# Optimization experiments

Measured on AMD Instinct MI355X. Metric: run time of the kernel, lower is better.

## Reference

```python
import jax, jax.numpy as jnp
import numpy as np

B, N, D = 64, 576, 768   # batch, num_patches (24x24), embed_dim
K = 1024                 # n_pairs
NUM_TARGETS = 2


def setup_inputs() -> dict:
    key = jax.random.key(0)
    k1, k2, k3, k4 = jax.random.split(key, 4)
    z = jax.random.normal(k1, (B, N, D), dtype=jnp.float32)
    indices = jax.random.randint(k2, (B, K, 2), 0, N, dtype=jnp.int64)
    # head params: nn.Linear(2*embed_dim, num_targets)
    W = jax.random.normal(k3, (2 * D, NUM_TARGETS), dtype=jnp.float32) * 0.02
    b_head = jax.random.normal(k4, (NUM_TARGETS,), dtype=jnp.float32) * 0.02
    return {"z": z, "indices": indices, "W": W, "b_head": b_head}


def reference(z, indices, W, b_head):
    b, n, d = z.shape
    k = indices.shape[1]
    # index_pairs: gather both patches of each pair -> [b, k, 2, d]
    batch_idx = jnp.arange(b)[:, None, None]            # [b,1,1]
    z_pairs = z[batch_idx, indices]                     # [b, k, 2, d]
    # pairwise_mlp head: concat pair along feature dim, tiny linear
    out = z_pairs.reshape(b, k, 2 * d) @ W + b_head     # [b, k, num_targets]
    return out, indices
```

## Files before the change

### kernel.cpp

```cpp
#include <hip/hip_runtime.h>

#define BB 64
#define NN 576
#define DD 768
#define KK 1024
#define ROWS (BB * NN)
#define PAIRS (BB * KK)

__device__ float4 g_P[ROWS];

__global__ __launch_bounds__(256) void partvit_proj(const float* __restrict__ z,
                                                    const float* __restrict__ W) {
    const int lane = threadIdx.x & 63;
    const int wid  = blockIdx.x * (blockDim.x >> 6) + (threadIdx.x >> 6);
    const int nw   = gridDim.x * (blockDim.x >> 6);

    const float2* __restrict__ W2 = (const float2*)W;
    float2 wa[3][4], wb[3][4];
#pragma unroll
    for (int j = 0; j < 3; ++j) {
#pragma unroll
        for (int c = 0; c < 4; ++c) {
            const int d = j * 256 + (lane << 2) + c;
            wa[j][c] = W2[d];
            wb[j][c] = W2[d + 768];
        }
    }

    const float4* __restrict__ z4 = (const float4*)z;

    for (int r = wid; r < ROWS; r += nw) {
        float a00 = 0.f, a01 = 0.f, a10 = 0.f, a11 = 0.f;
#pragma unroll
        for (int j = 0; j < 3; ++j) {
            const float4 v = z4[r * 192 + j * 64 + lane];
            a00 = fmaf(v.x, wa[j][0].x, a00);
            a00 = fmaf(v.y, wa[j][1].x, a00);
            a00 = fmaf(v.z, wa[j][2].x, a00);
            a00 = fmaf(v.w, wa[j][3].x, a00);
            a01 = fmaf(v.x, wa[j][0].y, a01);
            a01 = fmaf(v.y, wa[j][1].y, a01);
            a01 = fmaf(v.z, wa[j][2].y, a01);
            a01 = fmaf(v.w, wa[j][3].y, a01);
            a10 = fmaf(v.x, wb[j][0].x, a10);
            a10 = fmaf(v.y, wb[j][1].x, a10);
            a10 = fmaf(v.z, wb[j][2].x, a10);
            a10 = fmaf(v.w, wb[j][3].x, a10);
            a11 = fmaf(v.x, wb[j][0].y, a11);
            a11 = fmaf(v.y, wb[j][1].y, a11);
            a11 = fmaf(v.z, wb[j][2].y, a11);
            a11 = fmaf(v.w, wb[j][3].y, a11);
        }
#pragma unroll
        for (int off = 32; off > 0; off >>= 1) {
            a00 += __shfl_xor(a00, off, 64);
            a01 += __shfl_xor(a01, off, 64);
            a10 += __shfl_xor(a10, off, 64);
            a11 += __shfl_xor(a11, off, 64);
        }
        if (lane == 0) g_P[r] = make_float4(a00, a01, a10, a11);
    }
}

__global__ __launch_bounds__(256) void partvit_pairs(const int* __restrict__ idx,
                                                     const float* __restrict__ bh,
                                                     float* __restrict__ out) {
    const int t = blockIdx.x * blockDim.x + threadIdx.x;
    if (t >= PAIRS) return;
    const int2 id = ((const int2*)idx)[t];
    const int i0 = min(max(id.x, 0), NN - 1);
    const int i1 = min(max(id.y, 0), NN - 1);
    const int b = t >> 10;
    const float4 p0 = g_P[b * NN + i0];
    const float4 p1 = g_P[b * NN + i1];
    const float b0 = bh[0], b1 = bh[1];
    ((float2*)out)[t] = make_float2(p0.x + p1.z + b0, p0.y + p1.w + b1);
    ((float2*)out)[PAIRS + t] = make_float2((float)id.x, (float)id.y);
}

extern "C" void kernel_launch(void* const* d_in, const int* in_sizes, int n_in,
                              void* d_out, int out_size, void* d_ws, size_t ws_size,
                              hipStream_t stream) {
    const float* z   = (const float*)d_in[0];
    const int*   idx = (const int*)d_in[1];
    const float* W   = (const float*)d_in[2];
    const float* bh  = (const float*)d_in[3];
    float*       out = (float*)d_out;
    (void)d_ws; (void)ws_size;

    partvit_proj<<<1536, 256, 0, stream>>>(z, W);
    partvit_pairs<<<PAIRS / 256, 256, 0, stream>>>(idx, bh, out);
}
```

Baseline: 169.2 us.

## Fuse projection and pair gather into one per-batch kernel using shared memory

Result: slower. 188.0 us (+11.1%).

```diff
diff --git a/kernel.cpp b/kernel.cpp
--- a/kernel.cpp
+++ b/kernel.cpp
@@ -7,13 +7,15 @@
 #define ROWS (BB * NN)
 #define PAIRS (BB * KK)
 
-__device__ float4 g_P[ROWS];
-
-__global__ __launch_bounds__(256) void partvit_proj(const float* __restrict__ z,
-                                                    const float* __restrict__ W) {
+__global__ __launch_bounds__(1024) void partvit_fused(const float* __restrict__ z,
+                                                      const int* __restrict__ idx,
+                                                      const float* __restrict__ W,
+                                                      const float* __restrict__ bh,
+                                                      float* __restrict__ out) {
+    __shared__ float4 P[NN];
+    const int b    = blockIdx.x;
     const int lane = threadIdx.x & 63;
-    const int wid  = blockIdx.x * (blockDim.x >> 6) + (threadIdx.x >> 6);
-    const int nw   = gridDim.x * (blockDim.x >> 6);
+    const int wave = threadIdx.x >> 6;
 
     const float2* __restrict__ W2 = (const float2*)W;
     float2 wa[3][4], wb[3][4];
@@ -23,33 +25,57 @@
         for (int c = 0; c < 4; ++c) {
             const int d = j * 256 + (lane << 2) + c;
             wa[j][c] = W2[d];
-            wb[j][c] = W2[d + 768];
+            wb[j][c] = W2[d + DD];
         }
     }
 
-    const float4* __restrict__ z4 = (const float4*)z;
+    const float4* __restrict__ z4 = (const float4*)z + (size_t)b * NN * 192;
 
-    for (int r = wid; r < ROWS; r += nw) {
+    for (int r = wave; r < NN; r += 32) {
+        const int r2 = r + 16;
+        float4 v0[3], v1[3];
+#pragma unroll
+        for (int j = 0; j < 3; ++j) v0[j] = z4[r  * 192 + j * 64 + lane];
+#pragma unroll
+        for (int j = 0; j < 3; ++j) v1[j] = z4[r2 * 192 + j * 64 + lane];
+
         float a00 = 0.f, a01 = 0.f, a10 = 0.f, a11 = 0.f;
+        float c00 = 0.f, c01 = 0.f, c10 = 0.f, c11 = 0.f;
 #pragma unroll
         for (int j = 0; j < 3; ++j) {
-            const float4 v = z4[r * 192 + j * 64 + lane];
-            a00 = fmaf(v.x, wa[j][0].x, a00);
-            a00 = fmaf(v.y, wa[j][1].x, a00);
-            a00 = fmaf(v.z, wa[j][2].x, a00);
-            a00 = fmaf(v.w, wa[j][3].x, a00);
-            a01 = fmaf(v.x, wa[j][0].y, a01);
-            a01 = fmaf(v.y, wa[j][1].y, a01);
-            a01 = fmaf(v.z, wa[j][2].y, a01);
-            a01 = fmaf(v.w, wa[j][3].y, a01);
-            a10 = fmaf(v.x, wb[j][0].x, a10);
-            a10 = fmaf(v.y, wb[j][1].x, a10);
-            a10 = fmaf(v.z, wb[j][2].x, a10);
-            a10 = fmaf(v.w, wb[j][3].x, a10);
-            a11 = fmaf(v.x, wb[j][0].y, a11);
-            a11 = fmaf(v.y, wb[j][1].y, a11);
-            a11 = fmaf(v.z, wb[j][2].y, a11);
-            a11 = fmaf(v.w, wb[j][3].y, a11);
+            a00 = fmaf(v0[j].x, wa[j][0].x, a00);
+            a00 = fmaf(v0[j].y, wa[j][1].x, a00);
+            a00 = fmaf(v0[j].z, wa[j][2].x, a00);
+            a00 = fmaf(v0[j].w, wa[j][3].x, a00);
+            a01 = fmaf(v0[j].x, wa[j][0].y, a01);
+            a01 = fmaf(v0[j].y, wa[j][1].y, a01);
+            a01 = fmaf(v0[j].z, wa[j][2].y, a01);
+            a01 = fmaf(v0[j].w, wa[j][3].y, a01);
+            a10 = fmaf(v0[j].x, wb[j][0].x, a10);
+            a10 = fmaf(v0[j].y, wb[j][1].x, a10);
+            a10 = fmaf(v0[j].z, wb[j][2].x, a10);
+            a10 = fmaf(v0[j].w, wb[j][3].x, a10);
+            a11 = fmaf(v0[j].x, wb[j][0].y, a11);
+            a11 = fmaf(v0[j].y, wb[j][1].y, a11);
+            a11 = fmaf(v0[j].z, wb[j][2].y, a11);
+            a11 = fmaf(v0[j].w, wb[j][3].y, a11);
+
+            c00 = fmaf(v1[j].x, wa[j][0].x, c00);
+            c00 = fmaf(v1[j].y, wa[j][1].x, c00);
+            c00 = fmaf(v1[j].z, wa[j][2].x, c00);
+            c00 = fmaf(v1[j].w, wa[j][3].x, c00);
+            c01 = fmaf(v1[j].x, wa[j][0].y, c01);
+            c01 = fmaf(v1[j].y, wa[j][1].y, c01);
+            c01 = fmaf(v1[j].z, wa[j][2].y, c01);
+            c01 = fmaf(v1[j].w, wa[j][3].y, c01);
+            c10 = fmaf(v1[j].x, wb[j][0].x, c10);
+            c10 = fmaf(v1[j].y, wb[j][1].x, c10);
+            c10 = fmaf(v1[j].z, wb[j][2].x, c10);
+            c10 = fmaf(v1[j].w, wb[j][3].x, c10);
+            c11 = fmaf(v1[j].x, wb[j][0].y, c11);
+            c11 = fmaf(v1[j].y, wb[j][1].y, c11);
+            c11 = fmaf(v1[j].z, wb[j][2].y, c11);
+            c11 = fmaf(v1[j].w, wb[j][3].y, c11);
         }
 #pragma unroll
         for (int off = 32; off > 0; off >>= 1) {
@@ -57,22 +83,25 @@
             a01 += __shfl_xor(a01, off, 64);
             a10 += __shfl_xor(a10, off, 64);
             a11 += __shfl_xor(a11, off, 64);
+            c00 += __shfl_xor(c00, off, 64);
+            c01 += __shfl_xor(c01, off, 64);
+            c10 += __shfl_xor(c10, off, 64);
+            c11 += __shfl_xor(c11, off, 64);
         }
-        if (lane == 0) g_P[r] = make_float4(a00, a01, a10, a11);
+        if (lane == 0) {
+            P[r]  = make_float4(a00, a01, a10, a11);
+            P[r2] = make_float4(c00, c01, c10, c11);
+        }
     }
-}
 
-__global__ __launch_bounds__(256) void partvit_pairs(const int* __restrict__ idx,
-                                                     const float* __restrict__ bh,
-                                                     float* __restrict__ out) {
-    const int t = blockIdx.x * blockDim.x + threadIdx.x;
-    if (t >= PAIRS) return;
+    __syncthreads();
+
+    const int t = b * KK + (int)threadIdx.x;
     const int2 id = ((const int2*)idx)[t];
     const int i0 = min(max(id.x, 0), NN - 1);
     const int i1 = min(max(id.y, 0), NN - 1);
-    const int b = t >> 10;
-    const float4 p0 = g_P[b * NN + i0];
-    const float4 p1 = g_P[b * NN + i1];
+    const float4 p0 = P[i0];
+    const float4 p1 = P[i1];
     const float b0 = bh[0], b1 = bh[1];
     ((float2*)out)[t] = make_float2(p0.x + p1.z + b0, p0.y + p1.w + b1);
     ((float2*)out)[PAIRS + t] = make_float2((float)id.x, (float)id.y);
@@ -86,8 +115,7 @@
     const float* W   = (const float*)d_in[2];
     const float* bh  = (const float*)d_in[3];
     float*       out = (float*)d_out;
-    (void)d_ws; (void)ws_size;
+    (void)d_ws; (void)ws_size; (void)in_sizes; (void)n_in; (void)out_size;
 
-    partvit_proj<<<1536, 256, 0, stream>>>(z, W);
-    partvit_pairs<<<PAIRS / 256, 256, 0, stream>>>(idx, bh, out);
+    partvit_fused<<<BB, 1024, 0, stream>>>(z, idx, W, bh, out);
 }
```

## Fuse projection and pair gather into one kernel computing per-pair dot products

Applied to the files above, without the earlier changes.

New measurement: 187.2 us. +10.7%, slower.

```diff
diff --git a/kernel.cpp b/kernel.cpp
--- a/kernel.cpp
+++ b/kernel.cpp
@@ -7,75 +7,86 @@
 #define ROWS (BB * NN)
 #define PAIRS (BB * KK)
 
-__device__ float4 g_P[ROWS];
+#define NBLK 8192
+#define TPB  256
+#define PPB  8
 
-__global__ __launch_bounds__(256) void partvit_proj(const float* __restrict__ z,
-                                                    const float* __restrict__ W) {
+__global__ __launch_bounds__(TPB, 4)
+void partvit_direct(const float* __restrict__ z,
+                    const int* __restrict__ idx,
+                    const float* __restrict__ W,
+                    const float* __restrict__ bh,
+                    float* __restrict__ out) {
     const int lane = threadIdx.x & 63;
-    const int wid  = blockIdx.x * (blockDim.x >> 6) + (threadIdx.x >> 6);
-    const int nw   = gridDim.x * (blockDim.x >> 6);
+    const int wv   = threadIdx.x >> 6;
+
+    const int g  = (blockIdx.x & 7) * (NBLK / 8) + (blockIdx.x >> 3);
+    const int p0 = g * PPB + wv * 2;
+    const int p1 = p0 + 1;
+
+    const int2 id0 = ((const int2*)idx)[p0];
+    const int2 id1 = ((const int2*)idx)[p1];
+    const int bt  = p0 >> 10;
+    const int r00 = bt * NN + min(max(id0.x, 0), NN - 1);
+    const int r01 = bt * NN + min(max(id0.y, 0), NN - 1);
+    const int r10 = bt * NN + min(max(id1.x, 0), NN - 1);
+    const int r11 = bt * NN + min(max(id1.y, 0), NN - 1);
+
+    const float4* __restrict__ z4 = (const float4*)z;
+    float4 u0[3], u1[3], u2[3], u3[3];
+#pragma unroll
+    for (int j = 0; j < 3; ++j) u0[j] = z4[r00 * 192 + j * 64 + lane];
+#pragma unroll
+    for (int j = 0; j < 3; ++j) u1[j] = z4[r01 * 192 + j * 64 + lane];
+#pragma unroll
+    for (int j = 0; j < 3; ++j) u2[j] = z4[r10 * 192 + j * 64 + lane];
+#pragma unroll
+    for (int j = 0; j < 3; ++j) u3[j] = z4[r11 * 192 + j * 64 + lane];
 
     const float2* __restrict__ W2 = (const float2*)W;
-    float2 wa[3][4], wb[3][4];
+    const float* f0 = (const float*)u0;
+    const float* f1 = (const float*)u1;
+    const float* f2 = (const float*)u2;
+    const float* f3 = (const float*)u3;
+
+    float s00 = 0.f, s01 = 0.f, s10 = 0.f, s11 = 0.f;
 #pragma unroll
     for (int j = 0; j < 3; ++j) {
 #pragma unroll
         for (int c = 0; c < 4; ++c) {
             const int d = j * 256 + (lane << 2) + c;
-            wa[j][c] = W2[d];
-            wb[j][c] = W2[d + 768];
+            const float2 wA = W2[d];
+            const float2 wB = W2[d + DD];
+            const int e = j * 4 + c;
+            s00 = fmaf(f0[e], wA.x, s00);
+            s00 = fmaf(f1[e], wB.x, s00);
+            s01 = fmaf(f0[e], wA.y, s01);
+            s01 = fmaf(f1[e], wB.y, s01);
+            s10 = fmaf(f2[e], wA.x, s10);
+            s10 = fmaf(f3[e], wB.x, s10);
+            s11 = fmaf(f2[e], wA.y, s11);
+            s11 = fmaf(f3[e], wB.y, s11);
         }
     }
 
-    const float4* __restrict__ z4 = (const float4*)z;
+#pragma unroll
+    for (int off = 32; off > 0; off >>= 1) {
+        s00 += __shfl_xor(s00, off, 64);
+        s01 += __shfl_xor(s01, off, 64);
+        s10 += __shfl_xor(s10, off, 64);
+        s11 += __shfl_xor(s11, off, 64);
+    }
 
-    for (int r = wid; r < ROWS; r += nw) {
-        float a00 = 0.f, a01 = 0.f, a10 = 0.f, a11 = 0.f;
-#pragma unroll
-        for (int j = 0; j < 3; ++j) {
-            const float4 v = z4[r * 192 + j * 64 + lane];
-            a00 = fmaf(v.x, wa[j][0].x, a00);
-            a00 = fmaf(v.y, wa[j][1].x, a00);
-            a00 = fmaf(v.z, wa[j][2].x, a00);
-            a00 = fmaf(v.w, wa[j][3].x, a00);
-            a01 = fmaf(v.x, wa[j][0].y, a01);
-            a01 = fmaf(v.y, wa[j][1].y, a01);
-            a01 = fmaf(v.z, wa[j][2].y, a01);
-            a01 = fmaf(v.w, wa[j][3].y, a01);
-            a10 = fmaf(v.x, wb[j][0].x, a10);
-            a10 = fmaf(v.y, wb[j][1].x, a10);
-            a10 = fmaf(v.z, wb[j][2].x, a10);
-            a10 = fmaf(v.w, wb[j][3].x, a10);
-            a11 = fmaf(v.x, wb[j][0].y, a11);
-            a11 = fmaf(v.y, wb[j][1].y, a11);
-            a11 = fmaf(v.z, wb[j][2].y, a11);
-            a11 = fmaf(v.w, wb[j][3].y, a11);
-        }
-#pragma unroll
-        for (int off = 32; off > 0; off >>= 1) {
-            a00 += __shfl_xor(a00, off, 64);
-            a01 += __shfl_xor(a01, off, 64);
-            a10 += __shfl_xor(a10, off, 64);
-            a11 += __shfl_xor(a11, off, 64);
-        }
-        if (lane == 0) g_P[r] = make_float4(a00, a01, a10, a11);
+    const float b0 = bh[0], b1 = bh[1];
+    if (lane == 0) {
+        ((float2*)out)[p0] = make_float2(s00 + b0, s01 + b1);
+    } else if (lane == 1) {
+        ((float2*)out)[p1] = make_float2(s10 + b0, s11 + b1);
+    } else if (lane == 2) {
+        ((float2*)out)[PAIRS + p0] = make_float2((float)id0.x, (float)id0.y);
+    } else if (lane == 3) {
+        ((float2*)out)[PAIRS + p1] = make_float2((float)id1.x, (float)id1.y);
     }
-}
-
-__global__ __launch_bounds__(256) void partvit_pairs(const int* __restrict__ idx,
-                                                     const float* __restrict__ bh,
-                                                     float* __restrict__ out) {
-    const int t = blockIdx.x * blockDim.x + threadIdx.x;
-    if (t >= PAIRS) return;
-    const int2 id = ((const int2*)idx)[t];
-    const int i0 = min(max(id.x, 0), NN - 1);
-    const int i1 = min(max(id.y, 0), NN - 1);
-    const int b = t >> 10;
-    const float4 p0 = g_P[b * NN + i0];
-    const float4 p1 = g_P[b * NN + i1];
-    const float b0 = bh[0], b1 = bh[1];
-    ((float2*)out)[t] = make_float2(p0.x + p1.z + b0, p0.y + p1.w + b1);
-    ((float2*)out)[PAIRS + t] = make_float2((float)id.x, (float)id.y);
 }
 
 extern "C" void kernel_launch(void* const* d_in, const int* in_sizes, int n_in,
@@ -86,8 +97,7 @@
     const float* W   = (const float*)d_in[2];
     const float* bh  = (const float*)d_in[3];
     float*       out = (float*)d_out;
-    (void)d_ws; (void)ws_size;
+    (void)d_ws; (void)ws_size; (void)in_sizes; (void)n_in; (void)out_size;
 
-    partvit_proj<<<1536, 256, 0, stream>>>(z, W);
-    partvit_pairs<<<PAIRS / 256, 256, 0, stream>>>(idx, bh, out);
+    partvit_direct<<<NBLK, TPB, 0, stream>>>(z, idx, W, bh, out);
 }
```
